# Kernel tuning notes

Measured on AMD Instinct MI355X. Metric: run time of the kernel, lower is better.

## Reference

```python
import jax, jax.numpy as jnp
import numpy as np

D_HEADS = 2
MLP_H = 128
N_ENT = 100000
N_ROW = 30000
K_INST = 8
N_EDGE = 200000
N_REL = 200
IN_CH = 256
OUT_CH = 256


def _glorot(key, shape):
    fan_in = shape[0]
    return (jax.random.normal(key, shape, jnp.float32) / jnp.sqrt(jnp.float32(fan_in)))


def setup_inputs() -> dict:
    key = jax.random.key(0)
    ks = jax.random.split(key, 16)
    x = jax.random.normal(ks[0], (N_ENT, IN_CH), jnp.float32)
    ei0 = jax.random.randint(ks[1], (N_EDGE,), 0, N_ENT)   # target entities
    ei1 = jax.random.randint(ks[2], (N_EDGE,), 0, N_ROW)   # source instance rows
    edge_index = jnp.stack([ei0, ei1], 0).astype(jnp.int32)
    edge_order = jnp.arange(N_EDGE, dtype=jnp.int32)
    edge_type = jax.random.randint(ks[3], (N_EDGE,), 0, N_REL + 1).astype(jnp.int32)
    rel_embed = jax.random.normal(ks[4], (N_REL, IN_CH), jnp.float32)
    ids = jax.random.randint(ks[5], (N_ROW, K_INST), 0, N_ENT)
    pad = jax.random.uniform(ks[6], (N_ROW, K_INST)) < 0.4
    pad = pad.at[:, 0].set(False)  # each row keeps >=1 valid entry
    id2entity_instance = jnp.where(pad, -1, ids).astype(jnp.int32)
    return {
        'x': x, 'edge_index': edge_index, 'edge_order': edge_order,
        'edge_type': edge_type, 'rel_embed': rel_embed,
        'id2entity_instance': id2entity_instance,
        'W_in': _glorot(ks[7], (IN_CH, MLP_H * D_HEADS)), 'b_in': jnp.zeros((MLP_H * D_HEADS,), jnp.float32),
        'W_edge': _glorot(ks[8], (IN_CH, MLP_H * D_HEADS)), 'b_edge': jnp.zeros((MLP_H * D_HEADS,), jnp.float32),
        'W_sheaf': _glorot(ks[9], (2 * MLP_H, D_HEADS)), 'b_sheaf': jnp.zeros((D_HEADS,), jnp.float32),
        'W_conv': _glorot(ks[10], (MLP_H, MLP_H)), 'b_conv': jnp.zeros((MLP_H,), jnp.float32),
        'conv_bias': jnp.zeros((MLP_H,), jnp.float32),
        'w_rel': _glorot(ks[11], (IN_CH, OUT_CH)),
        'loop_rel': _glorot(ks[12], (1, IN_CH)),
        'mod_bias': jnp.zeros((OUT_CH,), jnp.float32),
        'bn_gamma': jnp.ones((OUT_CH,), jnp.float32), 'bn_beta': jnp.zeros((OUT_CH,), jnp.float32),
    }


def _forward(x, edge_index, edge_type, rel_embed, id2entity_instance,
             W_in, b_in, W_edge, b_edge, W_sheaf, b_sheaf,
             W_conv, b_conv, conv_bias, w_rel, loop_rel, mod_bias, bn_gamma, bn_beta):
    N, F = x.shape
    R = id2entity_instance.shape[0]
    E = edge_index.shape[1]
    d, H = D_HEADS, MLP_H
    # instance-dict embedding: padded gather (-1 wraps to the appended zero row) + masked mean
    x_add = jnp.concatenate([x, jnp.zeros((1, F), x.dtype)], 0)
    cnt = jnp.sum(id2entity_instance >= 0, axis=1, keepdims=True).astype(x.dtype)
    inst = jnp.sum(x_add[id2entity_instance], axis=1) / cnt          # (R, F)
    x_all = jnp.concatenate([x, inst], 0)                            # (N+R, F)
    Ntot = N + R
    # hypergraph incidence: each relational edge -> hyperedge with 2 nodes
    nodes = jnp.concatenate([edge_index[1] + N, edge_index[0]])      # (2E,)
    eids = jnp.concatenate([jnp.arange(E), jnp.arange(E)])           # (2E,)
    rel_full = jnp.concatenate([rel_embed, loop_rel], 0)             # (num_rels+1, F)
    # dual MLP projections (num_layers=1, InputNorm off -> plain linear)
    x_view = (x_all @ W_in + b_in).reshape(Ntot * d, H)
    e_view = (rel_full[edge_type] @ W_edge + b_edge).reshape(E * d, H)
    # sheaf builder (Diag, MLP_var1): mean over heads, gather, concat, linear, tanh
    x_mean = x_view.reshape(Ntot, d, H).mean(1)
    e_mean = e_view.reshape(E, d, H).mean(1)
    pair = jnp.concatenate([x_mean[nodes], e_mean[eids]], axis=-1)   # (2E, 2H)
    h_sheaf = jnp.tanh(pair @ W_sheaf + b_sheaf)                     # (2E, d)
    dr = jnp.arange(d)
    idx0 = (nodes[:, None] * d + dr).reshape(-1)                     # (2E*d,) node slots
    idx1 = (eids[:, None] * d + dr).reshape(-1)                      # (2E*d,) edge slots
    alpha = h_sheaf.reshape(-1)
    # HyperDiffusionDiagsheafConv (degree_norm, residual)
    h = x_view @ W_conv + b_conv                                     # (Ntot*d, H)
    Dn = jax.ops.segment_sum(alpha * alpha, idx0, num_segments=Ntot * d)
    Dinv = jnp.where(Dn > 0, 1.0 / Dn, 0.0)
    Be = jax.ops.segment_sum(jnp.ones_like(alpha), idx1, num_segments=E * d)
    Binv = jnp.where(Be > 0, 1.0 / Be, 0.0)
    ef = jax.ops.segment_sum((Binv[idx1] * alpha)[:, None] * h[idx0], idx1, num_segments=E * d)
    out = jax.ops.segment_sum((Dinv[idx0] * alpha)[:, None] * ef[idx1], idx0, num_segments=Ntot * d)
    out = out + conv_bias + h                                        # conv bias + residual
    out = jax.nn.elu(out).reshape(Ntot, d * H)
    out_ent = out[:N] + mod_bias
    # BatchNorm1d, training-mode statistics (biased var), eps=1e-5
    mu = out_ent.mean(0)
    var = out_ent.var(0)
    out_ent = (out_ent - mu) / jnp.sqrt(var + 1e-5) * bn_gamma + bn_beta
    r_out = (rel_full @ w_rel)[:-1]
    return out_ent, r_out


def reference(x, edge_index, edge_order, edge_type, rel_embed, id2entity_instance,
              W_in, b_in, W_edge, b_edge, W_sheaf, b_sheaf,
              W_conv, b_conv, conv_bias, w_rel, loop_rel, mod_bias, bn_gamma, bn_beta):
    # edge_order is accepted by the torch forward but unused
    return _forward(x, edge_index, edge_type, rel_embed, id2entity_instance,
                    W_in, b_in, W_edge, b_edge, W_sheaf, b_sheaf,
                    W_conv, b_conv, conv_bias, w_rel, loop_rel, mod_bias, bn_gamma, bn_beta)
```

## Files before the change

kernel.cpp:

```cpp
#include <hip/hip_runtime.h>
#include <stdint.h>

#define N_ENTC   100000
#define N_ROWC   30000
#define K_INSTC  8
#define N_EDGEC  200000
#define N_RELSC  200
#define NTOTC    (N_ENTC + N_ROWC)
#define CAPB     64

typedef _Float16 half8  __attribute__((ext_vector_type(8)));
typedef _Float16 half4v __attribute__((ext_vector_type(4)));
typedef float    float4v __attribute__((ext_vector_type(4)));

__global__ __launch_bounds__(256) void k_rel(
    const float* __restrict__ rel_embed, const float* __restrict__ loop_rel,
    const float* __restrict__ W_edge,    const float* __restrict__ b_edge,
    const float* __restrict__ W_sheaf,   const float* __restrict__ b_sheaf,
    const float* __restrict__ w_rel,
    float* __restrict__ s_edge_tab, float* __restrict__ out_rel)
{
  __shared__ float rel[256];
  __shared__ float eproj[256];
  __shared__ float em[128];
  int t = blockIdx.x;
  int c = threadIdx.x;
  rel[c] = (t < N_RELSC) ? rel_embed[t * 256 + c] : loop_rel[c];
  __syncthreads();
  float acc = b_edge[c];
  for (int k = 0; k < 256; ++k) acc += rel[k] * W_edge[k * 256 + c];
  eproj[c] = acc;
  __syncthreads();
  if (c < 128) em[c] = 0.5f * (eproj[c] + eproj[c + 128]);
  __syncthreads();
  if (c < 2) {
    float s = b_sheaf[c];
    for (int hh = 0; hh < 128; ++hh) s += em[hh] * W_sheaf[(128 + hh) * 2 + c];
    s_edge_tab[t * 2 + c] = s;
  }
  if (t < N_RELSC) {
    float ro = 0.f;
    for (int k = 0; k < 256; ++k) ro += rel[k] * w_rel[k * 256 + c];
    out_rel[t * 256 + c] = ro;
  }
}

__global__ __launch_bounds__(256) void k_fuse(
    const float* __restrict__ W_in,  const float* __restrict__ b_in,
    const float* __restrict__ W_conv, const float* __restrict__ b_conv,
    const float* __restrict__ W_sheaf,
    _Float16* __restrict__ Whi, _Float16* __restrict__ Wlo,
    float* __restrict__ b_comb, float* __restrict__ w_s)
{
  __shared__ float win[256];
  int k = blockIdx.x;
  int n = threadIdx.x;
  const float* src = (k < 256) ? (W_in + (size_t)k * 256) : b_in;
  win[n] = src[n];
  __syncthreads();
  int j = n >> 7, hh = n & 127;
  float acc = 0.f;
  for (int c = 0; c < 128; ++c)
    acc += win[j * 128 + c] * W_conv[c * 128 + hh];
  if (k < 256) {
    _Float16 hi = (_Float16)acc;
    _Float16 lo = (_Float16)(acc - (float)hi);
    int kt = k >> 5, g = (k >> 3) & 3, e = k & 7;
    int idx = ((kt * 16 + (n >> 4)) * 64 + (g * 16 + (n & 15))) * 8 + e;
    Whi[idx] = hi; Wlo[idx] = lo;
    if (n < 2) {
      float s = 0.f;
      for (int c2 = 0; c2 < 128; ++c2)
        s += 0.5f * (win[c2] + win[c2 + 128]) * W_sheaf[c2 * 2 + n];
      w_s[k * 2 + n] = s;
    }
  } else {
    b_comb[n] = acc + b_conv[hh];
    if (n < 2) {
      float s = 0.f;
      for (int c2 = 0; c2 < 128; ++c2)
        s += 0.5f * (win[c2] + win[c2 + 128]) * W_sheaf[c2 * 2 + n];
      w_s[512 + n] = s;
    }
  }
}

__global__ __launch_bounds__(256) void k_inst(
    const float* __restrict__ x, const int* __restrict__ ids,
    float* __restrict__ inst)
{
  int r = blockIdx.x;
  int c = threadIdx.x;
  float s = 0.f; int cnt = 0;
#pragma unroll
  for (int k = 0; k < K_INSTC; ++k) {
    int id = ids[r * K_INSTC + k];
    if (id >= 0) { s += x[(size_t)id * 256 + c]; cnt++; }
  }
  inst[(size_t)r * 256 + c] = s / (float)cnt;
}

__global__ __launch_bounds__(256) void k_snode(
    const float* __restrict__ x, const float* __restrict__ inst,
    const float* __restrict__ w_s, float* __restrict__ s_node)
{
  __shared__ float ws[514];
  int tid = threadIdx.x;
  for (int i = tid; i < 514; i += 256) ws[i] = w_s[i];
  __syncthreads();
  int r = tid >> 2, q = tid & 3;
  int row = blockIdx.x * 64 + r;
  if (row >= NTOTC) return;
  const float* src = (row < N_ENTC) ? (x + (size_t)row * 256)
                                    : (inst + (size_t)(row - N_ENTC) * 256);
  float s0 = 0.f, s1 = 0.f;
  int kbase = q * 64;
#pragma unroll
  for (int i = 0; i < 16; ++i) {
    float4 v = *(const float4*)(src + kbase + i * 4);
    int k2 = (kbase + i * 4) * 2;
    s0 += v.x * ws[k2 + 0] + v.y * ws[k2 + 2] + v.z * ws[k2 + 4] + v.w * ws[k2 + 6];
    s1 += v.x * ws[k2 + 1] + v.y * ws[k2 + 3] + v.z * ws[k2 + 5] + v.w * ws[k2 + 7];
  }
  s0 += __shfl_xor(s0, 1); s0 += __shfl_xor(s0, 2);
  s1 += __shfl_xor(s1, 1); s1 += __shfl_xor(s1, 2);
  if (q < 2) {
    float val = (q == 0) ? s0 : s1;
    s_node[(size_t)row * 2 + q] = val + ws[512 + q];
  }
}

__global__ __launch_bounds__(256, 3) void k_gemm(
    const float* __restrict__ x, const float* __restrict__ inst,
    const _Float16* __restrict__ Whi, const _Float16* __restrict__ Wlo,
    const float* __restrict__ b_comb,
    float* __restrict__ h)
{
  __shared__ _Float16 Ahi[64 * 64];
  __shared__ _Float16 Alo[64 * 64];

  int tid = threadIdx.x;
  int l = tid & 63;
  int w = tid >> 6;
  int row0 = blockIdx.x * 64;
  int g = l >> 4;
  int cn = l & 15;

  float4v acc[4][4];
#pragma unroll
  for (int a = 0; a < 4; ++a)
#pragma unroll
    for (int b = 0; b < 4; ++b) acc[a][b] = (float4v)(0.f);

  int rs = tid >> 4;
  int kb = (tid & 15) * 4;

  for (int ks = 0; ks < 4; ++ks) {
    int k0 = ks * 64;
#pragma unroll
    for (int i = 0; i < 4; ++i) {
      int r = rs + i * 16;
      int row = row0 + r;
      float4 v = make_float4(0.f, 0.f, 0.f, 0.f);
      if (row < N_ENTC) {
        v = *(const float4*)(x + (size_t)row * 256 + k0 + kb);
      } else if (row < NTOTC) {
        v = *(const float4*)(inst + (size_t)(row - N_ENTC) * 256 + k0 + kb);
      }
      half4v hv, lv;
      hv[0] = (_Float16)v.x; lv[0] = (_Float16)(v.x - (float)hv[0]);
      hv[1] = (_Float16)v.y; lv[1] = (_Float16)(v.y - (float)hv[1]);
      hv[2] = (_Float16)v.z; lv[2] = (_Float16)(v.z - (float)hv[2]);
      hv[3] = (_Float16)v.w; lv[3] = (_Float16)(v.w - (float)hv[3]);
      int idx = r * 64 + (((kb >> 3) ^ (r & 7)) << 3) + (kb & 7);
      *(half4v*)&Ahi[idx] = hv;
      *(half4v*)&Alo[idx] = lv;
    }
    __syncthreads();
#pragma unroll
    for (int kf = 0; kf < 2; ++kf) {
      int kt = ks * 2 + kf;
      half8 ah[4], al[4];
#pragma unroll
      for (int mt = 0; mt < 4; ++mt) {
        int row = mt * 16 + cn;
        int slot = (kf * 4 + g) ^ (cn & 7);
        int aidx = row * 64 + slot * 8;
        ah[mt] = *(const half8*)&Ahi[aidx];
        al[mt] = *(const half8*)&Alo[aidx];
      }
#pragma unroll
      for (int nt = 0; nt < 4; ++nt) {
        size_t boff = ((size_t)(kt * 16 + w * 4 + nt) * 64 + l) * 8;
        half8 bh = *(const half8*)(Whi + boff);
        half8 bl = *(const half8*)(Wlo + boff);
#pragma unroll
        for (int mt = 0; mt < 4; ++mt) {
          acc[mt][nt] = __builtin_amdgcn_mfma_f32_16x16x32_f16(ah[mt], bh, acc[mt][nt], 0, 0, 0);
          acc[mt][nt] = __builtin_amdgcn_mfma_f32_16x16x32_f16(al[mt], bh, acc[mt][nt], 0, 0, 0);
          acc[mt][nt] = __builtin_amdgcn_mfma_f32_16x16x32_f16(ah[mt], bl, acc[mt][nt], 0, 0, 0);
        }
      }
    }
    __syncthreads();
  }
#pragma unroll
  for (int nt = 0; nt < 4; ++nt) {
    int col = w * 64 + nt * 16 + cn;
    float bc = b_comb[col];
#pragma unroll
    for (int mt = 0; mt < 4; ++mt) {
      int rbase = row0 + mt * 16 + g * 4;
#pragma unroll
      for (int rr = 0; rr < 4; ++rr) {
        int row = rbase + rr;
        if (row < NTOTC)
          h[(size_t)row * 256 + col] = acc[mt][nt][rr] + bc;
      }
    }
  }
}

__global__ __launch_bounds__(256) void k_alpha(
    const int* __restrict__ ei0, const int* __restrict__ ei1,
    const int* __restrict__ etype,
    const float* __restrict__ s_node, const float* __restrict__ s_edge_tab,
    float* __restrict__ Dn, int* __restrict__ cnt,
    int* __restrict__ bR, float2* __restrict__ bC)
{
  int e = blockIdx.x * 256 + threadIdx.x;
  if (e >= N_EDGEC) return;
  int t = ei0[e], rI = ei1[e], ty = etype[e];
  float se0 = s_edge_tab[ty * 2 + 0], se1 = s_edge_tab[ty * 2 + 1];
  const float* snI = &s_node[(size_t)(N_ENTC + rI) * 2];
  const float* snT = &s_node[(size_t)t * 2];
  float a10 = tanhf(snI[0] + se0);
  float a11 = tanhf(snI[1] + se1);
  float a20 = tanhf(snT[0] + se0);
  float a21 = tanhf(snT[1] + se1);
  atomicAdd(&Dn[t * 2 + 0], a20 * a20);
  atomicAdd(&Dn[t * 2 + 1], a21 * a21);
  int pos = atomicAdd(&cnt[t], 1);
  if (pos < CAPB) {
    size_t slot = (size_t)t * CAPB + pos;
    bR[slot] = rI;
    bC[slot] = make_float2(0.5f * a10 * a20, 0.5f * a11 * a21);
  }
}

#define EPB 64
__global__ __launch_bounds__(256) void k_gather(
    float* h, const float* __restrict__ Dn,
    const int* __restrict__ cnt,
    const int* __restrict__ bR, const float2* __restrict__ bC,
    const float* __restrict__ conv_bias, const float* __restrict__ mod_bias,
    double* __restrict__ bnacc)
{
  int tid = threadIdx.x;
  int j = tid >> 7, hh = tid & 127;
  float cb = conv_bias[hh];
  float mb = mod_bias[tid];
  double s = 0.0, sq = 0.0;
  int t0 = blockIdx.x * EPB;
  for (int i = 0; i < EPB; ++i) {
    int t = t0 + i;
    if (t >= N_ENTC) break;
    int deg = cnt[t]; deg = (deg < CAPB) ? deg : CAPB;
    float dn = Dn[t * 2 + j];
    float dinv = (dn > 0.f) ? (1.0f / dn) : 0.f;
    float cross = 0.f;
    const int*    br = bR + (size_t)t * CAPB;
    const float2* bc = bC + (size_t)t * CAPB;
    for (int k = 0; k < deg; ++k) {
      int rI = br[k];
      float2 cc = bc[k];
      float c = (j == 0) ? cc.x : cc.y;
      cross += c * h[((size_t)(N_ENTC + rI) * 2 + j) * 128 + hh];
    }
    size_t idx = (size_t)t * 256 + tid;
    float ht = h[idx];
    float o = dinv * cross + ((dn > 0.f) ? 0.5f * ht : 0.f) + cb + ht;
    o = (o > 0.f) ? o : expm1f(o);
    o += mb;
    h[idx] = o;
    s += (double)o; sq += (double)o * (double)o;
  }
  atomicAdd(&bnacc[tid], s);
  atomicAdd(&bnacc[256 + tid], sq);
}

__global__ void k_bnstat(const double* __restrict__ bnacc,
                         const float* __restrict__ gamma, const float* __restrict__ beta,
                         float* __restrict__ ss)
{
  int c = threadIdx.x;
  double mu  = bnacc[c] / (double)N_ENTC;
  double var = bnacc[256 + c] / (double)N_ENTC - mu * mu;
  double istd = 1.0 / sqrt(var + 1e-5);
  float sc = (float)((double)gamma[c] * istd);
  float sh = (float)((double)beta[c] - mu * (double)sc);
  ss[c] = sc; ss[256 + c] = sh;
}

__global__ __launch_bounds__(256) void k_store(
    const float* __restrict__ prebn, const float* __restrict__ ss,
    float* __restrict__ out)
{
  size_t stride = (size_t)gridDim.x * 256 * 4;
  for (size_t i = ((size_t)blockIdx.x * 256 + threadIdx.x) * 4;
       i < (size_t)N_ENTC * 256; i += stride) {
    float4 a = *(const float4*)(prebn + i);
    int c = (int)(i & 255);
    float4 o;
    o.x = a.x * ss[c + 0] + ss[256 + c + 0];
    o.y = a.y * ss[c + 1] + ss[256 + c + 1];
    o.z = a.z * ss[c + 2] + ss[256 + c + 2];
    o.w = a.w * ss[c + 3] + ss[256 + c + 3];
    *(float4*)(out + i) = o;
  }
}

extern "C" void kernel_launch(void* const* d_in, const int* in_sizes, int n_in,
                              void* d_out, int out_size, void* d_ws, size_t ws_size,
                              hipStream_t stream)
{
  (void)in_sizes; (void)n_in; (void)out_size; (void)ws_size;

  const float* x         = (const float*)d_in[0];
  const int*   edge_idx  = (const int*)d_in[1];
  const int*   etype     = (const int*)d_in[3];
  const float* rel_embed = (const float*)d_in[4];
  const int*   ids       = (const int*)d_in[5];
  const float* W_in      = (const float*)d_in[6];
  const float* b_in      = (const float*)d_in[7];
  const float* W_edge    = (const float*)d_in[8];
  const float* b_edge    = (const float*)d_in[9];
  const float* W_sheaf   = (const float*)d_in[10];
  const float* b_sheaf   = (const float*)d_in[11];
  const float* W_conv    = (const float*)d_in[12];
  const float* b_conv    = (const float*)d_in[13];
  const float* conv_bias = (const float*)d_in[14];
  const float* w_rel     = (const float*)d_in[15];
  const float* loop_rel  = (const float*)d_in[16];
  const float* mod_bias  = (const float*)d_in[17];
  const float* bn_gamma  = (const float*)d_in[18];
  const float* bn_beta   = (const float*)d_in[19];

  const int* ei0 = edge_idx;
  const int* ei1 = edge_idx + N_EDGEC;

  char* ws = (char*)d_ws;
  const size_t OFF_H     = 0;
  const size_t OFF_DN    = OFF_H     + (size_t)NTOTC * 256 * 4;
  const size_t OFF_BN    = OFF_DN    + (size_t)N_ENTC * 2 * 4;
  const size_t OFF_CNT   = OFF_BN    + 4096;
  const size_t OFF_SNODE = OFF_CNT   + (size_t)N_ENTC * 4;
  const size_t OFF_SS    = OFF_SNODE + (size_t)NTOTC * 2 * 4;
  const size_t OFF_SEDGE = OFF_SS    + 2048;
  const size_t OFF_BIG   = OFF_SEDGE + 2048;
  const size_t OFF_WHI   = OFF_BIG   + (size_t)N_ROWC * 256 * 4;
  const size_t OFF_WLO   = OFF_WHI   + 131072;
  const size_t OFF_BC    = OFF_WLO   + 131072;
  const size_t OFF_WS    = OFF_BC    + 1024;
  const size_t OFF_BR    = OFF_BIG;
  const size_t OFF_BCC   = OFF_BR    + (size_t)N_ENTC * CAPB * 4;

  float*     h       = (float*)(ws + OFF_H);
  float*     Dn      = (float*)(ws + OFF_DN);
  double*    bnacc   = (double*)(ws + OFF_BN);
  int*       cnt     = (int*)(ws + OFF_CNT);
  float*     s_node  = (float*)(ws + OFF_SNODE);
  float*     ss      = (float*)(ws + OFF_SS);
  float*     s_edge  = (float*)(ws + OFF_SEDGE);
  float*     inst    = (float*)(ws + OFF_BIG);
  _Float16*  Whi     = (_Float16*)(ws + OFF_WHI);
  _Float16*  Wlo     = (_Float16*)(ws + OFF_WLO);
  float*     b_comb  = (float*)(ws + OFF_BC);
  float*     w_s     = (float*)(ws + OFF_WS);
  int*       bR      = (int*)(ws + OFF_BR);
  float2*    bC      = (float2*)(ws + OFF_BCC);

  float* out_ent = (float*)d_out;
  float* out_rel = (float*)d_out + (size_t)N_ENTC * 256;

  hipMemsetAsync(ws + OFF_DN, 0,
                 (size_t)N_ENTC * 2 * 4 + 4096 + (size_t)N_ENTC * 4, stream);

  k_rel<<<201, 256, 0, stream>>>(rel_embed, loop_rel, W_edge, b_edge,
                                 W_sheaf, b_sheaf, w_rel, s_edge, out_rel);
  k_fuse<<<257, 256, 0, stream>>>(W_in, b_in, W_conv, b_conv, W_sheaf,
                                  Whi, Wlo, b_comb, w_s);
  k_inst<<<N_ROWC, 256, 0, stream>>>(x, ids, inst);
  k_snode<<<(NTOTC + 63) / 64, 256, 0, stream>>>(x, inst, w_s, s_node);
  k_gemm<<<(NTOTC + 63) / 64, 256, 0, stream>>>(x, inst, Whi, Wlo, b_comb, h);

  k_alpha<<<(N_EDGEC + 255) / 256, 256, 0, stream>>>(ei0, ei1, etype,
                                                     s_node, s_edge,
                                                     Dn, cnt, bR, bC);
  k_gather<<<(N_ENTC + EPB - 1) / EPB, 256, 0, stream>>>(h, Dn, cnt, bR, bC,
                                                         conv_bias, mod_bias,
                                                         bnacc);
  k_bnstat<<<1, 256, 0, stream>>>(bnacc, bn_gamma, bn_beta, ss);
  k_store<<<8192, 256, 0, stream>>>(h, ss, out_ent);
}
```

Baseline: 594.1 us.

## Vectorize inst and gather kernels with float4, pack edge buckets into int4

k_inst now processes four rows per block with float4 loads and stores instead of one scalar channel per thread. The edge bucket arrays (row index plus two coefficients) are merged into one int4 record, so the gather loads one 16-byte entry per neighbor. k_gather gives each wavefront its own entity range, reads h in float4, and combines BatchNorm partial sums in shared memory before the atomics. The aim is fewer memory transactions and fewer instructions on the bandwidth-bound gather stages. The cost is a larger bucket footprint and a per-wave double reduction buffer in shared memory.

```diff
diff --git a/kernel.cpp b/kernel.cpp
--- a/kernel.cpp
+++ b/kernel.cpp
@@ -89,15 +89,24 @@
     const float* __restrict__ x, const int* __restrict__ ids,
     float* __restrict__ inst)
 {
-  int r = blockIdx.x;
-  int c = threadIdx.x;
-  float s = 0.f; int cnt = 0;
+  int tid = threadIdx.x;
+  int r = blockIdx.x * 4 + (tid >> 6);
+  int ch = (tid & 63) * 4;
+  if (r >= N_ROWC) return;
+  float4 s = make_float4(0.f, 0.f, 0.f, 0.f);
+  int cnt = 0;
 #pragma unroll
   for (int k = 0; k < K_INSTC; ++k) {
     int id = ids[r * K_INSTC + k];
-    if (id >= 0) { s += x[(size_t)id * 256 + c]; cnt++; }
-  }
-  inst[(size_t)r * 256 + c] = s / (float)cnt;
+    if (id >= 0) {
+      float4 v = *(const float4*)(x + (size_t)id * 256 + ch);
+      s.x += v.x; s.y += v.y; s.z += v.z; s.w += v.w;
+      cnt++;
+    }
+  }
+  float inv = 1.f / (float)cnt;
+  float4 o; o.x = s.x * inv; o.y = s.y * inv; o.z = s.z * inv; o.w = s.w * inv;
+  *(float4*)(inst + (size_t)r * 256 + ch) = o;
 }
 
 __global__ __launch_bounds__(256) void k_snode(
@@ -226,7 +235,7 @@
     const int* __restrict__ etype,
     const float* __restrict__ s_node, const float* __restrict__ s_edge_tab,
     float* __restrict__ Dn, int* __restrict__ cnt,
-    int* __restrict__ bR, float2* __restrict__ bC)
+    int4* __restrict__ bE)
 {
   int e = blockIdx.x * 256 + threadIdx.x;
   if (e >= N_EDGEC) return;
@@ -242,51 +251,74 @@
   atomicAdd(&Dn[t * 2 + 1], a21 * a21);
   int pos = atomicAdd(&cnt[t], 1);
   if (pos < CAPB) {
-    size_t slot = (size_t)t * CAPB + pos;
-    bR[slot] = rI;
-    bC[slot] = make_float2(0.5f * a10 * a20, 0.5f * a11 * a21);
+    int4 ee;
+    ee.x = rI; ee.y = 0;
+    ee.z = __float_as_int(0.5f * a10 * a20);
+    ee.w = __float_as_int(0.5f * a11 * a21);
+    bE[(size_t)t * CAPB + pos] = ee;
   }
 }
 
 #define EPB 64
 __global__ __launch_bounds__(256) void k_gather(
     float* h, const float* __restrict__ Dn,
-    const int* __restrict__ cnt,
-    const int* __restrict__ bR, const float2* __restrict__ bC,
+    const int* __restrict__ cnt, const int4* __restrict__ bE,
     const float* __restrict__ conv_bias, const float* __restrict__ mod_bias,
     double* __restrict__ bnacc)
 {
+  __shared__ double red[4][512];
   int tid = threadIdx.x;
-  int j = tid >> 7, hh = tid & 127;
-  float cb = conv_bias[hh];
-  float mb = mod_bias[tid];
-  double s = 0.0, sq = 0.0;
-  int t0 = blockIdx.x * EPB;
-  for (int i = 0; i < EPB; ++i) {
-    int t = t0 + i;
+  int wv = tid >> 6, l = tid & 63;
+  int ch = l * 4;
+  int j = l >> 5;
+  float4 cb = *(const float4*)(conv_bias + (ch & 127));
+  float4 mb = *(const float4*)(mod_bias + ch);
+  double s0 = 0, s1 = 0, s2 = 0, s3 = 0;
+  double q0 = 0, q1 = 0, q2 = 0, q3 = 0;
+  int tbase = blockIdx.x * EPB + wv * (EPB / 4);
+  for (int i = 0; i < EPB / 4; ++i) {
+    int t = tbase + i;
     if (t >= N_ENTC) break;
     int deg = cnt[t]; deg = (deg < CAPB) ? deg : CAPB;
     float dn = Dn[t * 2 + j];
     float dinv = (dn > 0.f) ? (1.0f / dn) : 0.f;
-    float cross = 0.f;
-    const int*    br = bR + (size_t)t * CAPB;
-    const float2* bc = bC + (size_t)t * CAPB;
+    float sf = (dn > 0.f) ? 1.5f : 1.0f;
+    float4 cr = make_float4(0.f, 0.f, 0.f, 0.f);
+    const int4* be = bE + (size_t)t * CAPB;
     for (int k = 0; k < deg; ++k) {
-      int rI = br[k];
-      float2 cc = bc[k];
-      float c = (j == 0) ? cc.x : cc.y;
-      cross += c * h[((size_t)(N_ENTC + rI) * 2 + j) * 128 + hh];
-    }
-    size_t idx = (size_t)t * 256 + tid;
-    float ht = h[idx];
-    float o = dinv * cross + ((dn > 0.f) ? 0.5f * ht : 0.f) + cb + ht;
-    o = (o > 0.f) ? o : expm1f(o);
-    o += mb;
-    h[idx] = o;
-    s += (double)o; sq += (double)o * (double)o;
-  }
-  atomicAdd(&bnacc[tid], s);
-  atomicAdd(&bnacc[256 + tid], sq);
+      int4 ee = be[k];
+      float c = (l < 32) ? __int_as_float(ee.z) : __int_as_float(ee.w);
+      float4 hv = *(const float4*)(h + (size_t)(N_ENTC + ee.x) * 256 + ch);
+      cr.x += c * hv.x; cr.y += c * hv.y; cr.z += c * hv.z; cr.w += c * hv.w;
+    }
+    size_t idx = (size_t)t * 256 + ch;
+    float4 ht = *(const float4*)(h + idx);
+    float4 o;
+    o.x = dinv * cr.x + sf * ht.x + cb.x;
+    o.y = dinv * cr.y + sf * ht.y + cb.y;
+    o.z = dinv * cr.z + sf * ht.z + cb.z;
+    o.w = dinv * cr.w + sf * ht.w + cb.w;
+    o.x = (o.x > 0.f) ? o.x : expm1f(o.x);
+    o.y = (o.y > 0.f) ? o.y : expm1f(o.y);
+    o.z = (o.z > 0.f) ? o.z : expm1f(o.z);
+    o.w = (o.w > 0.f) ? o.w : expm1f(o.w);
+    o.x += mb.x; o.y += mb.y; o.z += mb.z; o.w += mb.w;
+    *(float4*)(h + idx) = o;
+    s0 += (double)o.x; q0 += (double)o.x * (double)o.x;
+    s1 += (double)o.y; q1 += (double)o.y * (double)o.y;
+    s2 += (double)o.z; q2 += (double)o.z * (double)o.z;
+    s3 += (double)o.w; q3 += (double)o.w * (double)o.w;
+  }
+  red[wv][ch + 0] = s0; red[wv][ch + 1] = s1;
+  red[wv][ch + 2] = s2; red[wv][ch + 3] = s3;
+  red[wv][256 + ch + 0] = q0; red[wv][256 + ch + 1] = q1;
+  red[wv][256 + ch + 2] = q2; red[wv][256 + ch + 3] = q3;
+  __syncthreads();
+  double ssum = red[0][tid] + red[1][tid] + red[2][tid] + red[3][tid];
+  double qsum = red[0][256 + tid] + red[1][256 + tid]
+              + red[2][256 + tid] + red[3][256 + tid];
+  atomicAdd(&bnacc[tid], ssum);
+  atomicAdd(&bnacc[256 + tid], qsum);
 }
 
 __global__ void k_bnstat(const double* __restrict__ bnacc,
@@ -362,8 +394,7 @@
   const size_t OFF_WLO   = OFF_WHI   + 131072;
   const size_t OFF_BC    = OFF_WLO   + 131072;
   const size_t OFF_WS    = OFF_BC    + 1024;
-  const size_t OFF_BR    = OFF_BIG;
-  const size_t OFF_BCC   = OFF_BR    + (size_t)N_ENTC * CAPB * 4;
+  const size_t OFF_BE    = OFF_BIG;
 
   float*     h       = (float*)(ws + OFF_H);
   float*     Dn      = (float*)(ws + OFF_DN);
@@ -377,8 +408,7 @@
   _Float16*  Wlo     = (_Float16*)(ws + OFF_WLO);
   float*     b_comb  = (float*)(ws + OFF_BC);
   float*     w_s     = (float*)(ws + OFF_WS);
-  int*       bR      = (int*)(ws + OFF_BR);
-  float2*    bC      = (float2*)(ws + OFF_BCC);
+  int4*      bE      = (int4*)(ws + OFF_BE);
 
   float* out_ent = (float*)d_out;
   float* out_rel = (float*)d_out + (size_t)N_ENTC * 256;
@@ -390,14 +420,14 @@
                                  W_sheaf, b_sheaf, w_rel, s_edge, out_rel);
   k_fuse<<<257, 256, 0, stream>>>(W_in, b_in, W_conv, b_conv, W_sheaf,
                                   Whi, Wlo, b_comb, w_s);
-  k_inst<<<N_ROWC, 256, 0, stream>>>(x, ids, inst);
+  k_inst<<<(N_ROWC + 3) / 4, 256, 0, stream>>>(x, ids, inst);
   k_snode<<<(NTOTC + 63) / 64, 256, 0, stream>>>(x, inst, w_s, s_node);
   k_gemm<<<(NTOTC + 63) / 64, 256, 0, stream>>>(x, inst, Whi, Wlo, b_comb, h);
 
   k_alpha<<<(N_EDGEC + 255) / 256, 256, 0, stream>>>(ei0, ei1, etype,
                                                      s_node, s_edge,
-                                                     Dn, cnt, bR, bC);
-  k_gather<<<(N_ENTC + EPB - 1) / EPB, 256, 0, stream>>>(h, Dn, cnt, bR, bC,
+                                                     Dn, cnt, bE);
+  k_gather<<<(N_ENTC + EPB - 1) / EPB, 256, 0, stream>>>(h, Dn, cnt, bE,
                                                          conv_bias, mod_bias,
                                                          bnacc);
   k_bnstat<<<1, 256, 0, stream>>>(bnacc, bn_gamma, bn_beta, ss);
```

New measurement: 541.3 us. 1.1x faster.
